# Kernel optimization log

Hardware: AMD Instinct MI355X
Metric: run time of the kernel (lower is better)

## Reference

```python
import jax, jax.numpy as jnp
import numpy as np

N_NODES = 16500   # 100 battles x 165 hexes
N_EDGES = 100000  # per link type
K = 3             # number of link types (HeteroConv branches)
C_IN, C_HID, C_OUT = 170, 256, 256
GEN_EPS = 1e-7    # GENConv eps
BN_EPS = 1e-5     # BatchNorm1d eps


def setup_inputs() -> dict:
    key = jax.random.key(0)
    ki = iter(jax.random.split(key, 32))
    inp = {}
    inp["x"] = jax.random.normal(next(ki), (N_NODES, C_IN), jnp.float32)
    inp["edge_index"] = jax.random.randint(next(ki), (K, 2, N_EDGES), 0, N_NODES, dtype=jnp.int32)
    inp["edge_attr"] = jax.random.normal(next(ki), (K, N_EDGES, 1), jnp.float32)

    def uni(k, fan_in, shape):
        b = float(1.0 / np.sqrt(fan_in))
        return jax.random.uniform(k, shape, jnp.float32, -b, b)

    dims = [(C_IN, C_HID), (C_HID, C_HID), (C_HID, C_OUT)]
    for l, (ci, co) in enumerate(dims):
        inp[f"We{l}"] = uni(next(ki), 1, (K, 1, ci))          # edge encoder Linear(1, ci)
        inp[f"be{l}"] = jnp.zeros((K, ci), jnp.float32)
        inp[f"Wa{l}"] = uni(next(ki), ci, (K, ci, 2 * ci))     # MLP layer 1 (expansion=2)
        inp[f"ba{l}"] = jnp.zeros((K, 2 * ci), jnp.float32)
        inp[f"g{l}"] = jnp.ones((K, 2 * ci), jnp.float32)      # BatchNorm gamma
        inp[f"bt{l}"] = jnp.zeros((K, 2 * ci), jnp.float32)    # BatchNorm beta
        inp[f"Wb{l}"] = uni(next(ki), 2 * ci, (K, 2 * ci, co)) # MLP layer 2
        inp[f"bb{l}"] = jnp.zeros((K, co), jnp.float32)
    return inp


def _genconv(x, src, dst, ea, We, be, Wa, ba, g, bt, Wb, bb):
    """PyG GENConv (aggr='softmax', t=1, eps=1e-7, norm='batch') with self loops."""
    n = x.shape[0]
    loops = jnp.arange(n, dtype=src.dtype)
    src = jnp.concatenate([src, loops])
    dst = jnp.concatenate([dst, loops])
    ea = jnp.concatenate([ea, jnp.ones((n, ea.shape[1]), ea.dtype)], axis=0)
    e = ea @ We + be                           # [E+N, ci] edge encoder
    msg = jax.nn.relu(x[src] + e) + GEN_EPS    # [E+N, ci] message
    # per-destination, per-channel segment softmax aggregation
    mx = jax.ops.segment_max(msg, dst, num_segments=n)
    w = jnp.exp(msg - mx[dst])
    den = jax.ops.segment_sum(w, dst, num_segments=n)
    aggr = jax.ops.segment_sum(msg * w, dst, num_segments=n) / den
    out = aggr + x                             # residual with root node
    # MLP: Linear -> BatchNorm(train stats) -> ReLU -> Linear
    h = out @ Wa + ba
    mu = h.mean(axis=0)
    var = ((h - mu) ** 2).mean(axis=0)
    h = (h - mu) * jax.lax.rsqrt(var + BN_EPS) * g + bt
    h = jax.nn.relu(h)
    return h @ Wb + bb


_conv_k = jax.vmap(_genconv, in_axes=(None, 0, 0, 0, 0, 0, 0, 0, 0, 0, 0, 0))


def _forward(x, edge_index, edge_attr, layers):
    h = x
    for i, p in enumerate(layers):
        # HeteroConv: run GENConv per link type, sum-aggregate over types
        h = _conv_k(h, edge_index[:, 0], edge_index[:, 1], edge_attr, *p).sum(axis=0)
        if i < len(layers) - 1:
            h = jax.nn.leaky_relu(h, 0.01)
    return h


def reference(x, edge_index, edge_attr,
              We0, be0, Wa0, ba0, g0, bt0, Wb0, bb0,
              We1, be1, Wa1, ba1, g1, bt1, Wb1, bb1,
              We2, be2, Wa2, ba2, g2, bt2, Wb2, bb2):
    layers = [(We0, be0, Wa0, ba0, g0, bt0, Wb0, bb0),
              (We1, be1, Wa1, ba1, g1, bt1, Wb1, bb1),
              (We2, be2, Wa2, ba2, g2, bt2, Wb2, bb2)]
    return _forward(x, edge_index, edge_attr, layers)
```

## Files before the change

### kernel.cpp

```cpp
#include <hip/hip_runtime.h>
#include <math.h>

#define NN 16500
#define NP 16512
#define NE 100000
#define KT 3

typedef __attribute__((ext_vector_type(8))) short bf8_t;
typedef __attribute__((ext_vector_type(4))) float f4_t;

__device__ __forceinline__ unsigned short f2bf(float f) {
    unsigned int u = __float_as_uint(f);
    u += 0x7fffu + ((u >> 16) & 1u);
    return (unsigned short)(u >> 16);
}
__device__ __forceinline__ float bf2f(unsigned short h) {
    return __uint_as_float(((unsigned int)h) << 16);
}
__device__ __forceinline__ void gload16(unsigned short* lds, const unsigned short* g) {
    __builtin_amdgcn_global_load_lds(
        (const __attribute__((address_space(1))) void*)g,
        (__attribute__((address_space(3))) void*)lds, 16, 0, 0);
}


__global__ void deg_kernel(const int* __restrict__ ei, int* __restrict__ deg) {
    int t = blockIdx.x * blockDim.x + threadIdx.x;
    if (t >= KT * NE) return;
    int k = t / NE, e = t - k * NE;
    int d = ei[k * 2 * NE + NE + e];
    atomicAdd(&deg[k * NN + d], 1);
}

__global__ void scan_kernel(const int* __restrict__ deg, int* __restrict__ offs,
                            int* __restrict__ cursor) {
    int k = blockIdx.x;
    const int* dg = deg + k * NN;
    int* of = offs + k * (NN + 1);
    int* cu = cursor + k * NN;
    __shared__ int part[256];
    int tid = threadIdx.x;
    const int chunk = (NN + 255) / 256;
    int s0 = tid * chunk, s1 = min(NN, s0 + chunk);
    if (s0 > s1) s0 = s1;
    int sum = 0;
    for (int i = s0; i < s1; ++i) sum += dg[i];
    part[tid] = sum;
    __syncthreads();
    for (int off = 1; off < 256; off <<= 1) {
        int v = part[tid];
        int vp = (tid >= off) ? part[tid - off] : 0;
        __syncthreads();
        part[tid] = v + vp;
        __syncthreads();
    }
    int run = (tid == 0) ? 0 : part[tid - 1];
    for (int i = s0; i < s1; ++i) {
        of[i] = run; cu[i] = run;
        run += dg[i];
    }
    if (tid == 255) of[NN] = run;
}

__global__ void scatter_kernel(const int* __restrict__ ei, int* __restrict__ cursor,
                               int* __restrict__ eids) {
    int t = blockIdx.x * blockDim.x + threadIdx.x;
    if (t >= KT * NE) return;
    int k = t / NE, e = t - k * NE;
    int d = ei[k * 2 * NE + NE + e];
    int pos = atomicAdd(&cursor[k * NN + d], 1);
    eids[k * NE + pos] = e;
}


template<bool BF16X>
__device__ __forceinline__ void loadC(float out[2], const void* xv, int s, int c0, int ci) {
    if (BF16X) {
        unsigned int u = *(const unsigned int*)((const unsigned short*)xv + (size_t)s * ci + c0);
        out[0] = bf2f((unsigned short)(u & 0xffffu));
        out[1] = bf2f((unsigned short)(u >> 16));
    } else {
        out[0] = ((const float*)xv)[(size_t)s * ci + c0];
        out[1] = 0.f;
    }
}

template<bool BF16X>
__global__ __launch_bounds__(256) void aggr_kernel(
    const void* __restrict__ xv, const int* __restrict__ ei,
    const float* __restrict__ ea_all, const int* __restrict__ offs_all,
    const int* __restrict__ eids_all, const float* __restrict__ We_all,
    const float* __restrict__ be_all,
    unsigned short* __restrict__ out_hi, int ci, int kp)
{
    constexpr int CHPL = BF16X ? 2 : 1;
    int k = blockIdx.y;
    int wv = threadIdx.x >> 6, lane = threadIdx.x & 63;
    int d = blockIdx.x * 4 + wv;
    int c0 = blockIdx.z * 64 * CHPL + lane * CHPL;
    unsigned short* o = out_hi + (size_t)k * NP * kp;
    if (d >= NN) {
        if (c0 < kp) {
            if (BF16X) *(unsigned int*)(o + (size_t)d * kp + c0) = 0u;
            else o[(size_t)d * kp + c0] = 0;
        }
        return;
    }
    const int*   src  = ei + (size_t)k * 2 * NE;
    const float* ea   = ea_all + (size_t)k * NE;
    const int*   offs = offs_all + k * (NN + 1);
    const int*   eids = eids_all + (size_t)k * NE;
    const float* We   = We_all + (size_t)k * ci;
    const float* be   = be_all + (size_t)k * ci;

    bool act = c0 < ci;
    float w[CHPL], b[CHPL], xd[2] = {0.f, 0.f};
    #pragma unroll
    for (int e = 0; e < CHPL; ++e) {
        bool a = (c0 + e) < ci;
        w[e] = a ? We[c0 + e] : 0.f;
        b[e] = a ? be[c0 + e] : 0.f;
    }
    if (act) loadC<BF16X>(xd, xv, d, c0, ci);
    #pragma unroll
    for (int e = 0; e < CHPL; ++e) if ((c0 + e) >= ci) xd[e] = 0.f;

    float m[CHPL], den[CHPL], num[CHPL];
    #pragma unroll
    for (int e = 0; e < CHPL; ++e) {
        float mg = fmaxf(xd[e] + w[e] + b[e], 0.f);
        m[e] = mg; den[e] = 1.f; num[e] = mg;
    }

    int start = offs[d], end = offs[d + 1];
    for (int base = start; base < end; base += 64) {
        int cnt = min(64, end - base);
        int sv = 0; float av = 0.f;
        if (lane < cnt) {
            int e2 = eids[base + lane];
            sv = src[e2];
            av = ea[e2];
        }
        float xn[2] = {0.f, 0.f};
        int s0 = __shfl(sv, 0);
        if (act) loadC<BF16X>(xn, xv, s0, c0, ci);
        for (int j = 0; j < cnt; ++j) {
            float xc[2] = {xn[0], xn[1]};
            float a = __shfl(av, j);
            if (j + 1 < cnt) {
                int sn = __shfl(sv, j + 1);
                if (act) loadC<BF16X>(xn, xv, sn, c0, ci);
            }
            #pragma unroll
            for (int e = 0; e < CHPL; ++e) {
                float t = xc[e] + fmaf(a, w[e], b[e]);
                float mg = fmaxf(t, 0.f);
                float nm = fmaxf(m[e], mg);
                float mn = fminf(m[e], mg);
                float ex = __expf(mn - nm);
                bool keep = m[e] >= mg;
                float e0 = keep ? 1.f : ex;
                float e1 = keep ? ex : 1.f;
                den[e] = fmaf(den[e], e0, e1);
                num[e] = fmaf(num[e], e0, mg * e1);
                m[e] = nm;
            }
        }
    }
    if (c0 < kp) {
        unsigned short r[CHPL];
        #pragma unroll
        for (int e = 0; e < CHPL; ++e) {
            float v = ((c0 + e) < ci) ? (num[e] / den[e] + xd[e]) : 0.f;
            r[e] = f2bf(v);
        }
        if (BF16X)
            *(unsigned int*)(o + (size_t)d * kp + c0) =
                (unsigned)r[0] | ((unsigned)r[1] << 16);
        else
            o[(size_t)d * kp + c0] = r[0];
    }
}


struct SplitJob { const float* W; unsigned short* out; int kdim, ndim, np_, kp; };
struct SplitJobs { SplitJob j[6]; };

__global__ void split_all_kernel(SplitJobs jobs) {
    SplitJob jb = jobs.j[blockIdx.z];
    int idx = blockIdx.x * 256 + threadIdx.x;
    int total = KT * jb.np_ * jb.kp;
    if (idx >= total) return;
    int k = idx / (jb.np_ * jb.kp);
    int rem = idx - k * jb.np_ * jb.kp;
    int n = rem / jb.kp;
    int kk = rem - n * jb.kp;
    float v = (n < jb.ndim && kk < jb.kdim) ? jb.W[((size_t)k * jb.kdim + kk) * jb.ndim + n] : 0.f;
    jb.out[idx] = f2bf(v);
}


__global__ __launch_bounds__(256, 3) void gemm1_mfma(
    const unsigned short* __restrict__ A_hi,
    const unsigned short* __restrict__ B_hi,
    const float* __restrict__ bias_all, unsigned short* __restrict__ C_all,
    float* __restrict__ psum,
    int KP, int ldc, int Mv, int Nv)
{
    __shared__ unsigned short Ah[128 * 32];
    __shared__ unsigned short Bh[128 * 32];

    int z = blockIdx.z;
    int gxT = gridDim.x, gyT = gridDim.y;
    int NHP = gxT * 128;
    const unsigned short* Ahg = A_hi + (size_t)z * NP * KP;
    const unsigned short* Bhg = B_hi + (size_t)z * NHP * KP;
    const float* bias = bias_all + (size_t)z * Nv;
    unsigned short* C = C_all + (size_t)z * NP * ldc;

    int tid = threadIdx.x;
    int w = tid >> 6, l = tid & 63;
    int bm = blockIdx.y * 128, bn = blockIdx.x * 128;
    int lane15 = l & 15, quad = l >> 4;
    int wm = (w >> 1) * 64, wn = (w & 1) * 64;
    int srow = l & 15;
    int scol = (l >> 4) * 8;

    f4_t acc[4][4];
    #pragma unroll
    for (int i = 0; i < 4; ++i)
        #pragma unroll
        for (int j = 0; j < 4; ++j) { f4_t zz = {0.f,0.f,0.f,0.f}; acc[i][j] = zz; }

    size_t aoff0 = (size_t)(bm + 32 * w +  0 + srow) * KP + scol;
    size_t aoff1 = (size_t)(bm + 32 * w + 16 + srow) * KP + scol;
    size_t boff0 = (size_t)(bn + 32 * w +  0 + srow) * KP + scol;
    size_t boff1 = (size_t)(bn + 32 * w + 16 + srow) * KP + scol;
    int rb0 = 32 * w, rb1 = 32 * w + 16;
    int ta = (w >> 1) * 4, tb = (w & 1) * 4;

    for (int k0 = 0; k0 < KP; k0 += 32) {
        gload16(&Ah[rb0 * 32], Ahg + aoff0 + k0);
        gload16(&Ah[rb1 * 32], Ahg + aoff1 + k0);
        gload16(&Bh[rb0 * 32], Bhg + boff0 + k0);
        gload16(&Bh[rb1 * 32], Bhg + boff1 + k0);
        __syncthreads();

        bf8_t fa[4], fb[4];
        #pragma unroll
        for (int i = 0; i < 4; ++i) {
            fa[i] = *(const bf8_t*)&Ah[(ta + i) * 512 + l * 8];
            fb[i] = *(const bf8_t*)&Bh[(tb + i) * 512 + l * 8];
        }
        #pragma unroll
        for (int i = 0; i < 4; ++i)
            #pragma unroll
            for (int j = 0; j < 4; ++j)
                acc[i][j] = __builtin_amdgcn_mfma_f32_16x16x32_bf16(fa[i], fb[j], acc[i][j], 0, 0, 0);
        __syncthreads();
    }

    #pragma unroll
    for (int j = 0; j < 4; ++j) {
        int c = bn + wn + j * 16 + lane15;
        float bc = (c < Nv) ? bias[c] : 0.f;
        float s1 = 0.f, s2 = 0.f;
        #pragma unroll
        for (int i = 0; i < 4; ++i) {
            #pragma unroll
            for (int r5 = 0; r5 < 4; ++r5) {
                int r = bm + wm + i * 16 + quad * 4 + r5;
                float v = acc[i][j][r5] + bc;
                unsigned short q = f2bf(v);
                if (r < Mv && c < Nv) C[(size_t)r * ldc + c] = q;
                bool ok = (r < NN) && (c < Nv);
                float vq = ok ? bf2f(q) : 0.f;
                s1 += vq;
                s2 = fmaf(vq, vq, s2);
            }
        }
        s1 += __shfl_xor(s1, 16); s2 += __shfl_xor(s2, 16);
        s1 += __shfl_xor(s1, 32); s2 += __shfl_xor(s2, 32);
        if (quad == 0) {
            int wrow = w >> 1;
            int col = wn + j * 16 + lane15;
            size_t o = ((((size_t)z * gyT + blockIdx.y) * gxT + blockIdx.x) * 2 + wrow) * 256 + col * 2;
            float2 st = {s1, s2};
            *(float2*)&psum[o] = st;
        }
    }
}


__global__ __launch_bounds__(512) void finalize_kernel(
    const float* __restrict__ psum,
    const float* __restrict__ g_all, const float* __restrict__ bt_all,
    float* __restrict__ scale_all, float* __restrict__ shift_all,
    int hid, int gxT)
{
    int z = blockIdx.x;
    int c = threadIdx.x;
    if (c >= hid) return;
    int gx = c >> 7, col = c & 127;
    double s1 = 0.0, s2 = 0.0;
    for (int gy = 0; gy < NP / 128; ++gy) {
        size_t base = (((size_t)z * (NP / 128) + gy) * gxT + gx) * 2 * 256 + col * 2;
        float2 a  = *(const float2*)&psum[base];
        float2 b2 = *(const float2*)&psum[base + 256];
        s1 += (double)a.x + b2.x;
        s2 += (double)a.y + b2.y;
    }
    double mu = s1 / NN;
    double var = s2 / NN - mu * mu;
    if (var < 0.0) var = 0.0;
    float rs = (float)(1.0 / sqrt(var + 1e-5));
    float sc = rs * g_all[(size_t)z * hid + c];
    scale_all[(size_t)z * 512 + c] = sc;
    shift_all[(size_t)z * 512 + c] = bt_all[(size_t)z * hid + c] - (float)mu * sc;
}


__global__ __launch_bounds__(256, 3) void gemm2_mfma(
    const unsigned short* __restrict__ h_all, const float* __restrict__ scale_all,
    const float* __restrict__ shift_all,
    const unsigned short* __restrict__ B_hi,
    float* __restrict__ P_all, int KP, int hid, int Mv)
{
    __shared__ unsigned short Ah[128 * 32];
    __shared__ unsigned short Bh[128 * 32];

    int z = blockIdx.z;
    const unsigned short* hz = h_all + (size_t)z * NP * KP;
    const float* scl = scale_all + (size_t)z * 512;
    const float* shf = shift_all + (size_t)z * 512;
    const unsigned short* Bhg = B_hi + (size_t)z * 256 * KP;
    float* P = P_all + (size_t)z * NP * 256;

    int tid = threadIdx.x;
    int w = tid >> 6, l = tid & 63;
    int bm = blockIdx.y * 128, bn = blockIdx.x * 128;
    int lane15 = l & 15, quad = l >> 4;
    int wm = (w >> 1) * 64, wn = (w & 1) * 64;
    int srow = l & 15, scol = (l >> 4) * 8;

    f4_t acc[4][4];
    #pragma unroll
    for (int i = 0; i < 4; ++i)
        #pragma unroll
        for (int j = 0; j < 4; ++j) { f4_t zz = {0.f,0.f,0.f,0.f}; acc[i][j] = zz; }

    size_t boff0 = (size_t)(bn + 32 * w +  0 + srow) * KP + scol;
    size_t boff1 = (size_t)(bn + 32 * w + 16 + srow) * KP + scol;
    int rb0 = 32 * w, rb1 = 32 * w + 16;
    int ta = (w >> 1) * 4, tb = (w & 1) * 4;

    for (int k0 = 0; k0 < KP; k0 += 32) {
        gload16(&Bh[rb0 * 32], Bhg + boff0 + k0);
        gload16(&Bh[rb1 * 32], Bhg + boff1 + k0);

        #pragma unroll
        for (int sseg = 0; sseg < 2; ++sseg) {
            int L = sseg * 256 + tid;
            int chunk = (L >> 4) & 3;
            int grow = ((L >> 6) << 4) + (L & 15);
            int c = k0 + chunk * 8;
            uint4 hv = *(const uint4*)(hz + (size_t)(bm + grow) * KP + c);
            float4 s0 = *(const float4*)(scl + c);
            float4 s1 = *(const float4*)(scl + c + 4);
            float4 t0 = *(const float4*)(shf + c);
            float4 t1 = *(const float4*)(shf + c + 4);
            unsigned int uu[4] = {hv.x, hv.y, hv.z, hv.w};
            float ss[8] = {s0.x, s0.y, s0.z, s0.w, s1.x, s1.y, s1.z, s1.w};
            float tt[8] = {t0.x, t0.y, t0.z, t0.w, t1.x, t1.y, t1.z, t1.w};
            bf8_t hi8;
            #pragma unroll
            for (int e = 0; e < 8; ++e) {
                unsigned short hb = (e & 1) ? (unsigned short)(uu[e >> 1] >> 16)
                                            : (unsigned short)(uu[e >> 1] & 0xffffu);
                float x = bf2f(hb);
                float val = (c + e < hid) ? fmaxf(fmaf(x, ss[e], tt[e]), 0.f) : 0.f;
                hi8[e] = (short)f2bf(val);
            }
            *(bf8_t*)&Ah[L * 8] = hi8;
        }
        __syncthreads();

        bf8_t fa[4], fb[4];
        #pragma unroll
        for (int i = 0; i < 4; ++i) {
            fa[i] = *(const bf8_t*)&Ah[(ta + i) * 512 + l * 8];
            fb[i] = *(const bf8_t*)&Bh[(tb + i) * 512 + l * 8];
        }
        #pragma unroll
        for (int i = 0; i < 4; ++i)
            #pragma unroll
            for (int j = 0; j < 4; ++j)
                acc[i][j] = __builtin_amdgcn_mfma_f32_16x16x32_bf16(fa[i], fb[j], acc[i][j], 0, 0, 0);
        __syncthreads();
    }

    #pragma unroll
    for (int i = 0; i < 4; ++i)
        #pragma unroll
        for (int j = 0; j < 4; ++j) {
            int c = bn + wn + j * 16 + lane15;
            #pragma unroll
            for (int r5 = 0; r5 < 4; ++r5) {
                int r = bm + wm + i * 16 + quad * 4 + r5;
                if (r < Mv)
                    P[(size_t)r * 256 + c] = acc[i][j][r5];
            }
        }
}


__global__ __launch_bounds__(256) void reduce_kernel(
    const float* __restrict__ P, const float* __restrict__ bb,
    float* __restrict__ outf, unsigned short* __restrict__ outb,
    int leaky, int as_bf16)
{
    int idx = blockIdx.x * 256 + threadIdx.x;
    if (idx >= NN * 64) return;
    int r = idx >> 6, c = (idx & 63) * 4;
    const float4 p0 = *(const float4*)&P[((size_t)0 * NP + r) * 256 + c];
    const float4 p1 = *(const float4*)&P[((size_t)1 * NP + r) * 256 + c];
    const float4 p2 = *(const float4*)&P[((size_t)2 * NP + r) * 256 + c];
    const float4 b0 = *(const float4*)&bb[c];
    const float4 b1 = *(const float4*)&bb[256 + c];
    const float4 b2 = *(const float4*)&bb[512 + c];
    float v[4] = {p0.x + p1.x + p2.x + b0.x + b1.x + b2.x,
                  p0.y + p1.y + p2.y + b0.y + b1.y + b2.y,
                  p0.z + p1.z + p2.z + b0.z + b1.z + b2.z,
                  p0.w + p1.w + p2.w + b0.w + b1.w + b2.w};
    if (leaky) {
        #pragma unroll
        for (int e = 0; e < 4; ++e) v[e] = (v[e] > 0.f) ? v[e] : 0.01f * v[e];
    }
    if (as_bf16) {
        unsigned int o0 = (unsigned int)f2bf(v[0]) | ((unsigned int)f2bf(v[1]) << 16);
        unsigned int o1 = (unsigned int)f2bf(v[2]) | ((unsigned int)f2bf(v[3]) << 16);
        uint2 o = {o0, o1};
        *(uint2*)&outb[(size_t)r * 256 + c] = o;
    } else {
        float4 o = {v[0], v[1], v[2], v[3]};
        *(float4*)&outf[(size_t)r * 256 + c] = o;
    }
}


extern "C" void kernel_launch(void* const* d_in, const int* in_sizes, int n_in,
                              void* d_out, int out_size, void* d_ws, size_t ws_size,
                              hipStream_t stream)
{
    const float* x  = (const float*)d_in[0];
    const int*   ei = (const int*)d_in[1];
    const float* ea = (const float*)d_in[2];

    char* w = (char*)d_ws;
    auto alloc = [&](size_t bytes) {
        char* p = w;
        w += (bytes + 255) & ~(size_t)255;
        return p;
    };
    int* deg    = (int*)alloc((size_t)KT * NN * 4);
    int* offs   = (int*)alloc((size_t)KT * (NN + 1) * 4);
    int* cursor = (int*)alloc((size_t)KT * NN * 4);
    int* eids   = (int*)alloc((size_t)KT * NE * 4);
    unsigned short* a1_hi = (unsigned short*)alloc((size_t)KT * NP * 256 * 2);
    unsigned short* h3 = (unsigned short*)alloc((size_t)KT * NP * 512 * 2);
    float* partial = (float*)alloc((size_t)KT * NP * 256 * 4);
    unsigned short* bta_l[3];
    unsigned short* btb_l[3];
    for (int l = 0; l < 3; ++l) {
        bta_l[l] = (unsigned short*)alloc((size_t)KT * 512 * 256 * 2);
        btb_l[l] = (unsigned short*)alloc((size_t)KT * 256 * 512 * 2);
    }
    float* psum = (float*)alloc((size_t)KT * (NP / 128) * 4 * 2 * 256 * 4);
    float* scale3 = (float*)alloc((size_t)KT * 512 * 4);
    float* shift3 = (float*)alloc((size_t)KT * 512 * 4);
    unsigned short* bufA = (unsigned short*)alloc((size_t)NN * 256 * 2);
    unsigned short* bufB = (unsigned short*)alloc((size_t)NN * 256 * 2);

    hipMemsetAsync(deg, 0, (size_t)KT * NN * 4, stream);
    int net = KT * NE;
    deg_kernel<<<(net + 255) / 256, 256, 0, stream>>>(ei, deg);
    scan_kernel<<<KT, 256, 0, stream>>>(deg, offs, cursor);
    scatter_kernel<<<(net + 255) / 256, 256, 0, stream>>>(ei, cursor, eids);

    SplitJobs jobs;
    int maxtot = 0;
    for (int l = 0; l < 3; ++l) {
        int ci  = (l == 0) ? 170 : 256;
        int KP1 = (ci + 31) / 32 * 32;
        int hid = 2 * ci;
        int NHP = (hid + 127) / 128 * 128;
        int KP2 = (hid + 31) / 32 * 32;
        jobs.j[2 * l]     = { (const float*)d_in[3 + 8 * l + 2], bta_l[l], ci,  hid, NHP, KP1 };
        jobs.j[2 * l + 1] = { (const float*)d_in[3 + 8 * l + 6], btb_l[l], hid, 256, 256, KP2 };
        maxtot = max(maxtot, KT * NHP * KP1);
        maxtot = max(maxtot, KT * 256 * KP2);
    }
    dim3 gsp((maxtot + 255) / 256, 1, 6);
    split_all_kernel<<<gsp, 256, 0, stream>>>(jobs);

    const void* hin = x;
    for (int l = 0; l < 3; ++l) {
        int ci  = (l == 0) ? 170 : 256;
        int KP1 = (ci + 31) / 32 * 32;
        int hid = 2 * ci;
        int NHP = (hid + 127) / 128 * 128;
        int KP2 = (hid + 31) / 32 * 32;
        const float* We = (const float*)d_in[3 + 8 * l + 0];
        const float* be = (const float*)d_in[3 + 8 * l + 1];
        const float* ba = (const float*)d_in[3 + 8 * l + 3];
        const float* g  = (const float*)d_in[3 + 8 * l + 4];
        const float* bt = (const float*)d_in[3 + 8 * l + 5];
        const float* bb = (const float*)d_in[3 + 8 * l + 7];

        if (l == 0) {
            dim3 ga(NP / 4, KT, 3);
            aggr_kernel<false><<<ga, 256, 0, stream>>>(hin, ei, ea, offs, eids, We, be,
                                                       a1_hi, ci, KP1);
        } else {
            dim3 ga(NP / 4, KT, 2);
            aggr_kernel<true><<<ga, 256, 0, stream>>>(hin, ei, ea, offs, eids, We, be,
                                                      a1_hi, ci, KP1);
        }

        dim3 g1(NHP / 128, NP / 128, KT);
        gemm1_mfma<<<g1, 256, 0, stream>>>(a1_hi, bta_l[l], ba, h3, psum, KP1, KP2, NN, hid);

        finalize_kernel<<<KT, 512, 0, stream>>>(psum, g, bt, scale3, shift3, hid, NHP / 128);

        dim3 g2(2, NP / 128, KT);
        gemm2_mfma<<<g2, 256, 0, stream>>>(h3, scale3, shift3, btb_l[l],
                                           partial, KP2, hid, NP);

        unsigned short* outb = (l == 0) ? bufA : bufB;
        reduce_kernel<<<(NN * 64 + 255) / 256, 256, 0, stream>>>(
            partial, bb, (float*)d_out, outb, (l < 2) ? 1 : 0, (l < 2) ? 1 : 0);

        hin = (l < 2) ? (const void*)outb : nullptr;
    }
}
```

Measured before the change: 766.8 us.

## Process four channels per lane in aggregation, removing channel-split grid dimension

The edge aggregation kernel now handles four channels per lane, so one wavefront covers a whole destination row and the z grid dimension that split channels across blocks is gone. Each destination's edge list, source indices and edge attributes are therefore read once instead of two or three times. Row loads are widened to 8-byte or float2 accesses, the edge loop is unrolled by two with two rows prefetched, and channel count is a compile-time constant. This cuts redundant index traffic and launch count, but each lane does more serial work and holds more registers, which may lower latency hiding on high-degree nodes.

```diff
diff --git a/kernel.cpp b/kernel.cpp
--- a/kernel.cpp
+++ b/kernel.cpp
@@ -73,64 +73,89 @@
 }
 
 
-template<bool BF16X>
-__device__ __forceinline__ void loadC(float out[2], const void* xv, int s, int c0, int ci) {
+template<int CI, bool BF16X>
+__device__ __forceinline__ void loadrow4(float out[4], const void* xv, int s, int c0) {
     if (BF16X) {
-        unsigned int u = *(const unsigned int*)((const unsigned short*)xv + (size_t)s * ci + c0);
-        out[0] = bf2f((unsigned short)(u & 0xffffu));
-        out[1] = bf2f((unsigned short)(u >> 16));
+        const unsigned short* xb = (const unsigned short*)xv;
+        uint2 u = *(const uint2*)(xb + (size_t)s * CI + c0);
+        out[0] = bf2f((unsigned short)(u.x & 0xffffu));
+        out[1] = bf2f((unsigned short)(u.x >> 16));
+        out[2] = bf2f((unsigned short)(u.y & 0xffffu));
+        out[3] = bf2f((unsigned short)(u.y >> 16));
     } else {
-        out[0] = ((const float*)xv)[(size_t)s * ci + c0];
-        out[1] = 0.f;
-    }
-}
-
-template<bool BF16X>
+        const float* p = (const float*)xv + (size_t)s * CI + c0;
+        if (c0 + 4 <= CI) {
+            float2 ab = *(const float2*)p;
+            float2 cd = *(const float2*)(p + 2);
+            out[0] = ab.x; out[1] = ab.y; out[2] = cd.x; out[3] = cd.y;
+        } else {
+            #pragma unroll
+            for (int e = 0; e < 4; ++e) out[e] = (c0 + e < CI) ? p[e] : 0.f;
+        }
+    }
+}
+
+template<int CI, bool BF16X>
 __global__ __launch_bounds__(256) void aggr_kernel(
     const void* __restrict__ xv, const int* __restrict__ ei,
     const float* __restrict__ ea_all, const int* __restrict__ offs_all,
     const int* __restrict__ eids_all, const float* __restrict__ We_all,
     const float* __restrict__ be_all,
-    unsigned short* __restrict__ out_hi, int ci, int kp)
+    unsigned short* __restrict__ out_hi)
 {
-    constexpr int CHPL = BF16X ? 2 : 1;
+    constexpr int KP = (CI + 31) / 32 * 32;
     int k = blockIdx.y;
     int wv = threadIdx.x >> 6, lane = threadIdx.x & 63;
     int d = blockIdx.x * 4 + wv;
-    int c0 = blockIdx.z * 64 * CHPL + lane * CHPL;
-    unsigned short* o = out_hi + (size_t)k * NP * kp;
+    int c0 = lane * 4;
+    unsigned short* o = out_hi + (size_t)k * NP * KP;
     if (d >= NN) {
-        if (c0 < kp) {
-            if (BF16X) *(unsigned int*)(o + (size_t)d * kp + c0) = 0u;
-            else o[(size_t)d * kp + c0] = 0;
-        }
+        if (c0 < KP) { uint2 z = {0u, 0u}; *(uint2*)(o + (size_t)d * KP + c0) = z; }
         return;
     }
     const int*   src  = ei + (size_t)k * 2 * NE;
     const float* ea   = ea_all + (size_t)k * NE;
     const int*   offs = offs_all + k * (NN + 1);
     const int*   eids = eids_all + (size_t)k * NE;
-    const float* We   = We_all + (size_t)k * ci;
-    const float* be   = be_all + (size_t)k * ci;
-
-    bool act = c0 < ci;
-    float w[CHPL], b[CHPL], xd[2] = {0.f, 0.f};
-    #pragma unroll
-    for (int e = 0; e < CHPL; ++e) {
-        bool a = (c0 + e) < ci;
+    const float* We   = We_all + (size_t)k * CI;
+    const float* be   = be_all + (size_t)k * CI;
+
+    constexpr bool ACT_ALL = (64 * 4 == KP) && (CI == KP);
+    bool act = ACT_ALL || (c0 < CI);
+    float w[4], b[4], xd[4] = {0.f, 0.f, 0.f, 0.f};
+    #pragma unroll
+    for (int e = 0; e < 4; ++e) {
+        bool a = (c0 + e) < CI;
         w[e] = a ? We[c0 + e] : 0.f;
         b[e] = a ? be[c0 + e] : 0.f;
     }
-    if (act) loadC<BF16X>(xd, xv, d, c0, ci);
-    #pragma unroll
-    for (int e = 0; e < CHPL; ++e) if ((c0 + e) >= ci) xd[e] = 0.f;
-
-    float m[CHPL], den[CHPL], num[CHPL];
-    #pragma unroll
-    for (int e = 0; e < CHPL; ++e) {
+    if (act) loadrow4<CI, BF16X>(xd, xv, d, c0);
+    #pragma unroll
+    for (int e = 0; e < 4; ++e) if ((c0 + e) >= CI) xd[e] = 0.f;
+
+    float m[4], den[4], num[4];
+    #pragma unroll
+    for (int e = 0; e < 4; ++e) {
         float mg = fmaxf(xd[e] + w[e] + b[e], 0.f);
         m[e] = mg; den[e] = 1.f; num[e] = mg;
     }
+
+    auto step = [&](const float xc[4], float a) {
+        #pragma unroll
+        for (int e = 0; e < 4; ++e) {
+            float t = xc[e] + fmaf(a, w[e], b[e]);
+            float mg = fmaxf(t, 0.f);
+            float nm = fmaxf(m[e], mg);
+            float mn = fminf(m[e], mg);
+            float ex = __expf(mn - nm);
+            bool keep = m[e] >= mg;
+            float e0 = keep ? 1.f : ex;
+            float e1 = keep ? ex : 1.f;
+            den[e] = fmaf(den[e], e0, e1);
+            num[e] = fmaf(num[e], e0, mg * e1);
+            m[e] = nm;
+        }
+    };
 
     int start = offs[d], end = offs[d + 1];
     for (int base = start; base < end; base += 64) {
@@ -141,44 +166,46 @@
             sv = src[e2];
             av = ea[e2];
         }
-        float xn[2] = {0.f, 0.f};
-        int s0 = __shfl(sv, 0);
-        if (act) loadC<BF16X>(xn, xv, s0, c0, ci);
-        for (int j = 0; j < cnt; ++j) {
-            float xc[2] = {xn[0], xn[1]};
-            float a = __shfl(av, j);
-            if (j + 1 < cnt) {
-                int sn = __shfl(sv, j + 1);
-                if (act) loadC<BF16X>(xn, xv, sn, c0, ci);
+        float x0[4] = {0.f,0.f,0.f,0.f}, x1[4] = {0.f,0.f,0.f,0.f};
+        {
+            int sA = __shfl(sv, 0);
+            if (act) loadrow4<CI, BF16X>(x0, xv, sA, c0);
+        }
+        if (cnt > 1) {
+            int sB = __shfl(sv, 1);
+            if (act) loadrow4<CI, BF16X>(x1, xv, sB, c0);
+        }
+        int j = 0;
+        for (; j + 1 < cnt; j += 2) {
+            float a0 = __shfl(av, j), a1 = __shfl(av, j + 1);
+            float tA[4] = {x0[0], x0[1], x0[2], x0[3]};
+            float tB[4] = {x1[0], x1[1], x1[2], x1[3]};
+            if (j + 2 < cnt) {
+                int sn = __shfl(sv, j + 2);
+                if (act) loadrow4<CI, BF16X>(x0, xv, sn, c0);
             }
-            #pragma unroll
-            for (int e = 0; e < CHPL; ++e) {
-                float t = xc[e] + fmaf(a, w[e], b[e]);
-                float mg = fmaxf(t, 0.f);
-                float nm = fmaxf(m[e], mg);
-                float mn = fminf(m[e], mg);
-                float ex = __expf(mn - nm);
-                bool keep = m[e] >= mg;
-                float e0 = keep ? 1.f : ex;
-                float e1 = keep ? ex : 1.f;
-                den[e] = fmaf(den[e], e0, e1);
-                num[e] = fmaf(num[e], e0, mg * e1);
-                m[e] = nm;
+            if (j + 3 < cnt) {
+                int sn = __shfl(sv, j + 3);
+                if (act) loadrow4<CI, BF16X>(x1, xv, sn, c0);
             }
-        }
-    }
-    if (c0 < kp) {
-        unsigned short r[CHPL];
-        #pragma unroll
-        for (int e = 0; e < CHPL; ++e) {
-            float v = ((c0 + e) < ci) ? (num[e] / den[e] + xd[e]) : 0.f;
+            step(tA, a0);
+            step(tB, a1);
+        }
+        if (j < cnt) {
+            float a0 = __shfl(av, j);
+            step(x0, a0);
+        }
+    }
+    if (c0 < KP) {
+        unsigned short r[4];
+        #pragma unroll
+        for (int e = 0; e < 4; ++e) {
+            float v = ((c0 + e) < CI) ? (num[e] / den[e] + xd[e]) : 0.f;
             r[e] = f2bf(v);
         }
-        if (BF16X)
-            *(unsigned int*)(o + (size_t)d * kp + c0) =
-                (unsigned)r[0] | ((unsigned)r[1] << 16);
-        else
-            o[(size_t)d * kp + c0] = r[0];
+        uint2 pk = {(unsigned)r[0] | ((unsigned)r[1] << 16),
+                    (unsigned)r[2] | ((unsigned)r[3] << 16)};
+        *(uint2*)(o + (size_t)d * KP + c0) = pk;
     }
 }
 
@@ -517,15 +544,13 @@
         const float* bt = (const float*)d_in[3 + 8 * l + 5];
         const float* bb = (const float*)d_in[3 + 8 * l + 7];
 
-        if (l == 0) {
-            dim3 ga(NP / 4, KT, 3);
-            aggr_kernel<false><<<ga, 256, 0, stream>>>(hin, ei, ea, offs, eids, We, be,
-                                                       a1_hi, ci, KP1);
-        } else {
-            dim3 ga(NP / 4, KT, 2);
-            aggr_kernel<true><<<ga, 256, 0, stream>>>(hin, ei, ea, offs, eids, We, be,
-                                                      a1_hi, ci, KP1);
-        }
+        dim3 ga(NP / 4, KT);
+        if (l == 0)
+            aggr_kernel<170, false><<<ga, 256, 0, stream>>>(hin, ei, ea, offs, eids,
+                                                            We, be, a1_hi);
+        else
+            aggr_kernel<256, true><<<ga, 256, 0, stream>>>(hin, ei, ea, offs, eids,
+                                                           We, be, a1_hi);
 
         dim3 g1(NHP / 128, NP / 128, KT);
         gemm1_mfma<<<g1, 256, 0, stream>>>(a1_hi, bta_l[l], ba, h3, psum, KP1, KP2, NN, hid);
```

After: 697.9 us. -9.0%, faster.
